# Kernel tuning notes

Hardware: AMD Instinct MI355X
Metric: run time of the kernel (lower is better)

## Reference

```python
import math
import jax, jax.numpy as jnp
import numpy as np

B, V, N, D, H = 8, 8, 1000, 256, 8
KS = D // H
TANH_CLIP = 10.0
F_NODE = 8   # node dynamic features incl. is_to_be_delivered flag
F_VEH = 8


def setup_inputs() -> dict:
    key = jax.random.key(0)
    ks = jax.random.split(key, 13)
    s = 1.0 / math.sqrt(D)
    mask = jax.random.uniform(ks[8], (B, V, N)) > 0.3
    mask = mask.at[:, :, 0].set(True)  # guarantee at least one feasible action
    return {
        'node_embeddings': jax.random.normal(ks[0], (B, N, D), jnp.float32),
        'fixed_context': jax.random.normal(ks[1], (B, 1, D), jnp.float32),
        'prev_node_embeddings': jax.random.normal(ks[2], (B, V, D), jnp.float32),
        'node_dynamic_features': jax.random.uniform(ks[3], (B, V, N, F_NODE), jnp.float32),
        'vehicle_dynamic_features': jax.random.uniform(ks[4], (B, V, F_VEH), jnp.float32),
        'glimpse_V_static': jax.random.normal(ks[5], (H, B, 1, N, KS), jnp.float32),
        'glimpse_K_static': jax.random.normal(ks[6], (H, B, 1, N, KS), jnp.float32),
        'logit_K_static': jax.random.normal(ks[7], (B, 1, N, D), jnp.float32),
        'feasibility_mask': mask,
        'pcs_weight': jax.random.normal(ks[9], (D, D + F_VEH), jnp.float32) * s,
        'pns1_weight': jax.random.normal(ks[10], (3 * D, F_NODE - 1), jnp.float32) * s,
        'pns2_weight': jax.random.normal(ks[11], (3 * D, 3 * D + 1), jnp.float32) * s,
        'po_weight': jax.random.normal(ks[12], (D, D), jnp.float32) * s,
    }


def _make_heads(x):
    # [B,V,N,D] -> [H,B,V,N,KS]  (matches unsqueeze/view/permute in torch code)
    b, v, n, _ = x.shape
    return x.reshape(b, v, n, H, KS).transpose(3, 0, 1, 2, 4)


def reference(node_embeddings, fixed_context, prev_node_embeddings,
              node_dynamic_features, vehicle_dynamic_features,
              glimpse_V_static, glimpse_K_static, logit_K_static,
              feasibility_mask, pcs_weight, pns1_weight, pns2_weight, po_weight):
    b, n, d = node_embeddings.shape
    v = vehicle_dynamic_features.shape[1]

    # projected current vehicle state
    cvs = jnp.concatenate([prev_node_embeddings, vehicle_dynamic_features], axis=-1)  # [B,V,D+Fv]
    proj_cvs = cvs @ pcs_weight.T                                                     # [B,V,D]

    # node dynamic embeddings (hypernet linears)
    flag = node_dynamic_features[..., -1:]
    feats = node_dynamic_features[..., :-1]
    x = feats @ pns1_weight.T                                   # [B,V,N,3D]
    x_ = jnp.concatenate([x, flag], axis=-1) @ pns2_weight.T    # [B,V,N,3D]
    nde = x + x_
    gVd, gKd, lKd = jnp.split(nde, 3, axis=-1)                  # each [B,V,N,D]

    glimpse_V = glimpse_V_static + _make_heads(gVd)             # [H,B,V,N,KS]
    glimpse_K = glimpse_K_static + _make_heads(gKd)             # [H,B,V,N,KS]
    logit_K = logit_K_static + lKd                              # [B,V,N,D]

    query = fixed_context + proj_cvs                            # [B,V,D]
    gQ = query.reshape(b, v, H, 1, KS).transpose(2, 0, 1, 3, 4)  # [H,B,V,1,KS]

    logmask = jnp.log(feasibility_mask.astype(jnp.float32))     # 0 / -inf, [B,V,N]

    compat = jnp.einsum('hbvqk,hbvnk->hbvqn', gQ, glimpse_K) / math.sqrt(KS)
    compat = compat + logmask[None, :, :, None, :]              # [H,B,V,1,N]

    # softmax over all (vehicle, node) pairs jointly
    attn = jax.nn.softmax(compat.reshape(H, b, v * n), axis=-1).reshape(compat.shape)
    heads = jnp.einsum('hbvqn,hbvnk->hbvqk', attn, glimpse_V)   # [H,B,V,1,KS]

    concated = heads.transpose(1, 2, 3, 0, 4).reshape(b, v, 1, d)
    final_Q = concated @ po_weight.T                            # [B,V,1,D]

    logits = jnp.einsum('bvqd,bvnd->bvqn', final_Q, logit_K) / math.sqrt(d)
    logits = jnp.tanh(logits) * TANH_CLIP
    logits = logits[:, :, 0, :] + logmask                       # [B,V,N]
    logits = logits.reshape(b, v * n)
    probs = jax.nn.softmax(logits, axis=1)

    # greedy (eval-mode) selection
    op = jnp.argmax(probs, axis=-1)
    prob = jnp.max(probs, axis=-1)
    logprob = jnp.log(prob)
    entropy = -jnp.sum(prob * logprob)
    selected_vecs = (op // n).astype(jnp.int64)
    selected_nodes = op % n
    return selected_vecs, selected_nodes, logprob, entropy
```

## Files before the change

kernel.cpp:

```cpp
#include <hip/hip_runtime.h>
#include <math.h>

#define OFF_MW     0
#define OFF_QUERY  6144
#define OFF_CSUMP  22528
#define OFF_HSTATP 23040
#define OFF_S8P    154112
#define OFF_FQ     186880
#define OFF_LQM    203264
#define OFF_EXPSP  203776
#define OFF_PACKP  204032
#define OFF_DONE   204544
#define OFF_BM     204545

__device__ inline float waveSum(float v){
  #pragma unroll
  for (int o = 32; o > 0; o >>= 1) v += __shfl_down(v, o, 64);
  return v;
}
__device__ inline unsigned long long waveMaxU(unsigned long long v){
  #pragma unroll
  for (int o = 32; o > 0; o >>= 1) {
    unsigned long long w = __shfl_down(v, o, 64);
    v = (w > v) ? w : v;
  }
  return v;
}
__device__ inline unsigned encF(float f){
  unsigned u = __float_as_uint(f);
  return (u & 0x80000000u) ? ~u : (u | 0x80000000u);
}
__device__ inline float decF(unsigned u){
  return (u & 0x80000000u) ? __uint_as_float(u & 0x7fffffffu)
                           : __uint_as_float(~u);
}

__global__ __launch_bounds__(256) void k_prep(
    const float* __restrict__ pns1, const float* __restrict__ pns2,
    const float* __restrict__ prev, const float* __restrict__ veh,
    const float* __restrict__ fixedc, const float* __restrict__ pcs,
    const void* __restrict__ maskp, float* __restrict__ W)
{
  int blk = blockIdx.x, tid = threadIdx.x;
  float* mw     = W + OFF_MW;
  float* queryp = W + OFF_QUERY;

  if (blk < 768) {
    int i = blk;
    __shared__ float red[28];
    const float* row = pns2 + (size_t)i * 769;
    float acc[7] = {0.f,0.f,0.f,0.f,0.f,0.f,0.f};
    #pragma unroll
    for (int t = 0; t < 3; t++) {
      int j = tid + 256 * t;
      float r = row[j];
      const float* w = pns1 + j * 7;
      #pragma unroll
      for (int f = 0; f < 7; f++) acc[f] += r * w[f];
    }
    #pragma unroll
    for (int f = 0; f < 7; f++) {
      float v = waveSum(acc[f]);
      if ((tid & 63) == 0) red[(tid >> 6) * 7 + f] = v;
    }
    __syncthreads();
    if (tid < 7) {
      float s = red[tid] + red[7 + tid] + red[14 + tid] + red[21 + tid];
      mw[i * 8 + tid] = pns1[i * 7 + tid] + s;
    } else if (tid == 7) {
      mw[i * 8 + 7] = row[768];
    }
  } else if (blk < 832) {
    int bv = blk - 768;
    __shared__ __align__(16) float cvs[264];
    cvs[tid] = prev[(size_t)bv * 256 + tid];
    if (tid < 8) cvs[256 + tid] = veh[bv * 8 + tid];
    __syncthreads();
    int b = bv >> 3;
    float a = fixedc[b * 256 + tid];
    const float4* c4 = (const float4*)cvs;
    const float4* w4 = (const float4*)(pcs + (size_t)tid * 264);
    #pragma unroll 8
    for (int k = 0; k < 66; k++) {
      float4 cv = c4[k], wv = w4[k];
      a += cv.x*wv.x + cv.y*wv.y + cv.z*wv.z + cv.w*wv.w;
    }
    queryp[(size_t)bv * 256 + tid] = a;
  } else {
    __shared__ unsigned hits[4];
    const unsigned char* mb = (const unsigned char*)maskp;
    bool hit = (tid > 0) && ((tid & 3) != 0) && (mb[tid] != 0);
    unsigned long long bal = __ballot(hit);
    if ((tid & 63) == 0) hits[tid >> 6] = (bal != 0ull) ? 1u : 0u;
    __syncthreads();
    if (tid == 0) {
      ((unsigned*)(W + OFF_BM))[0] = hits[0] | hits[1] | hits[2] | hits[3];
      ((unsigned*)(W + OFF_DONE))[0] = 0u;
    }
  }
}

__global__ __launch_bounds__(256) void k_attn(
    const float* __restrict__ node_dyn, const float* __restrict__ gVs,
    const float* __restrict__ gKs, const void* __restrict__ maskp,
    float* __restrict__ W)
{
  const int blk = blockIdx.x, tid = threadIdx.x;
  const int b = blk & 7, c = (blk >> 3) & 7, h = blk >> 6;
  const int n0 = c * 125;
  const float* mw     = W + OFF_MW;
  const float* queryp = W + OFF_QUERY;
  float* csum_p  = W + OFF_CSUMP;
  float* hstat_p = W + OFF_HSTATP;
  float* s8_p    = W + OFF_S8P;
  const int bytemode = *(const int*)(W + OFF_BM);

  __shared__ __align__(16) float p[1000];
  __shared__ __align__(16) float gq[256];
  __shared__ float mwK[256];
  __shared__ float qmk[64];
  __shared__ float red4[4];
  __shared__ float s8part[256];
  __shared__ __align__(16) float gvL[4000];
  __shared__ __align__(16) float gkL[4500];
  __shared__ __align__(16) float ndL[8000];

  gq[tid]  = queryp[(size_t)(b * 8 + (tid >> 5)) * 256 + h * 32 + (tid & 31)];
  mwK[tid] = mw[(256 + h * 32) * 8 + tid];
  __syncthreads();
  if (tid < 64) {
    int v = tid >> 3, f = tid & 7;
    float a = 0.f;
    #pragma unroll
    for (int k = 0; k < 32; k++)
      a += gq[v * 32 + k] * mwK[k * 8 + f];
    qmk[tid] = a;
  }
  {
    const float4* gv4 = (const float4*)(gVs + ((size_t)(h * 8 + b) * 1000 + n0) * 32);
    const float4* gk4 = (const float4*)(gKs + ((size_t)(h * 8 + b) * 1000 + n0) * 32);
    for (int idx = tid; idx < 1000; idx += 256) {
      int row = idx >> 3, c4 = idx & 7;
      ((float4*)gvL)[idx] = gv4[idx];
      ((float4*)(gkL + row * 36))[c4] = gk4[idx];
    }
  }
  __syncthreads();

  float tsum = 0.f;
  for (int e = tid; e < 1000; e += 256) {
    int v = e / 125;
    int i = e - v * 125;
    int n = n0 + i;
    int bvn = (b * 8 + v) * 1000 + n;
    const float4* nd4 = (const float4*)(node_dyn + (size_t)bvn * 8);
    float4 ndA = nd4[0], ndB = nd4[1];
    ((float4*)ndL)[e * 2]     = ndA;
    ((float4*)ndL)[e * 2 + 1] = ndB;
    const float4* gk4 = (const float4*)(gkL + i * 36);
    const float4* gq4 = (const float4*)(gq + v * 32);
    float s = 0.f;
    #pragma unroll
    for (int k4 = 0; k4 < 8; k4++) {
      float4 g = gk4[k4], q = gq4[k4];
      s += g.x*q.x + g.y*q.y + g.z*q.z + g.w*q.w;
    }
    const float* qm = qmk + v * 8;
    float dyn = ndA.x*qm[0] + ndA.y*qm[1] + ndA.z*qm[2] + ndA.w*qm[3]
              + ndB.x*qm[4] + ndB.y*qm[5] + ndB.z*qm[6] + ndB.w*qm[7];
    bool on = bytemode ? (((const unsigned char*)maskp)[bvn] != 0)
                       : (((const int*)maskp)[bvn] != 0);
    float cc = (s + dyn) * 0.17677669529663687f + (on ? 0.f : -INFINITY);
    float pv = __expf(cc);
    p[e] = pv;
    tsum += pv;
  }
  tsum = waveSum(tsum);
  if ((tid & 63) == 0) red4[tid >> 6] = tsum;
  __syncthreads();
  if (tid == 0) csum_p[blk] = red4[0] + red4[1] + red4[2] + red4[3];

  if (tid < 64) {
    int v = tid >> 3, kq = tid & 7;
    const float* pr = p + v * 125;
    const float4* gv4 = ((const float4*)gvL) + kq;
    float4 a = make_float4(0.f, 0.f, 0.f, 0.f);
    #pragma unroll 5
    for (int i = 0; i < 125; i++) {
      float pi = pr[i];
      float4 g = gv4[i * 8];
      a.x += pi * g.x; a.y += pi * g.y; a.z += pi * g.z; a.w += pi * g.w;
    }
    ((float4*)(hstat_p + (size_t)blk * 256))[tid] = a;
  } else {
    int j0 = tid - 64;
    #pragma unroll
    for (int rep = 0; rep < 2; rep++) {
      int t = j0 + rep * 192;
      if (t < 256) {
        int sidx = t & 3, vf = t >> 2;
        int v = vf >> 3, f = vf & 7;
        int i0 = sidx * 32;
        int iN = (sidx == 3) ? 29 : 32;
        const float* nd = ndL + ((size_t)(v * 125 + i0)) * 8 + f;
        const float* pr = p + v * 125 + i0;
        float a = 0.f;
        for (int i = 0; i < iN; i++) a += pr[i] * nd[i * 8];
        s8part[sidx * 64 + vf] = a;
      }
    }
  }
  __syncthreads();
  if (tid < 64)
    s8_p[(size_t)blk * 64 + tid] = s8part[tid] + s8part[64 + tid]
                                 + s8part[128 + tid] + s8part[192 + tid];
}

__global__ __launch_bounds__(256) void k_fq(
    const float* __restrict__ po, float* __restrict__ W)
{
  const int blk = blockIdx.x, tid = threadIdx.x;
  const int b = blk & 7, v = (blk >> 3) & 7;
  const float* mwgV    = W + OFF_MW;
  const float* mwgL    = W + OFF_MW + 512 * 8;
  const float* csum_p  = W + OFF_CSUMP;
  const float* hstat_p = W + OFF_HSTATP;
  const float* s8_p    = W + OFF_S8P;
  float* fqg  = W + OFF_FQ;
  float* lqmg = W + OFF_LQM;

  __shared__ __align__(16) float hstatF[2048];
  __shared__ float csumF[8];
  __shared__ float s8F[512];
  __shared__ __align__(16) float cl[256];
  __shared__ float fql[256];
  __shared__ float part[256];

  #pragma unroll
  for (int h2 = 0; h2 < 8; h2++) {
    float s = 0.f;
    #pragma unroll
    for (int cc = 0; cc < 8; cc++)
      s += hstat_p[(size_t)((h2 << 6) | (cc << 3) | b) * 256 + tid];
    hstatF[h2 * 256 + tid] = s;
  }
  if (tid < 8) {
    float s = 0.f;
    #pragma unroll
    for (int cc = 0; cc < 8; cc++) s += csum_p[(tid << 6) | (cc << 3) | b];
    csumF[tid] = s;
  }
  #pragma unroll
  for (int idx = tid; idx < 512; idx += 256) {
    int h2 = idx >> 6, vf = idx & 63;
    float s = 0.f;
    #pragma unroll
    for (int cc = 0; cc < 8; cc++)
      s += s8_p[(size_t)((h2 << 6) | (cc << 3) | b) * 64 + vf];
    s8F[idx] = s;
  }
  __syncthreads();
  {
    int h2 = tid >> 5, k2 = tid & 31;
    float dyn = 0.f;
    const float* s8pp = s8F + h2 * 64 + v * 8;
    const float* mwp = mwgV + tid * 8;
    #pragma unroll
    for (int f = 0; f < 8; f++) dyn += s8pp[f] * mwp[f];
    cl[tid] = (hstatF[h2 * 256 + v * 32 + k2] + dyn) / csumF[h2];
  }
  __syncthreads();
  {
    float a = 0.f;
    const float4* c4 = (const float4*)cl;
    const float4* w4 = (const float4*)(po + (size_t)tid * 256);
    #pragma unroll 8
    for (int e = 0; e < 64; e++) {
      float4 cv = c4[e], wv = w4[e];
      a += cv.x*wv.x + cv.y*wv.y + cv.z*wv.z + cv.w*wv.w;
    }
    fql[tid] = a;
    fqg[(size_t)(b * 8 + v) * 256 + tid] = a;
  }
  __syncthreads();
  {
    int cc2 = tid >> 3, f = tid & 7;
    float s = 0.f;
    for (int d = cc2 * 8; d < cc2 * 8 + 8; d++) s += fql[d] * mwgL[d * 8 + f];
    part[tid] = s;
  }
  __syncthreads();
  if (tid < 8) {
    float s = 0.f;
    for (int cc2 = 0; cc2 < 32; cc2++) s += part[cc2 * 8 + tid];
    lqmg[(b * 8 + v) * 8 + tid] = s;
  }
}

__global__ __launch_bounds__(256) void k_logits(
    const float* __restrict__ lKs, const float* __restrict__ node_dyn,
    const void* __restrict__ maskp, float* __restrict__ W,
    float* __restrict__ out)
{
  const int blk = blockIdx.x, tid = threadIdx.x;
  const int b = blk & 7, slice = blk >> 3;
  const int nn = tid >> 3, v = tid & 7;
  const int n = slice * 32 + nn;
  const bool valid = (n < 1000);
  const int n_c = valid ? n : 999;
  const float* fqg  = W + OFF_FQ;
  const float* lqmg = W + OFF_LQM;
  float* expsum_p = W + OFF_EXPSP;
  unsigned long long* packed_p = (unsigned long long*)(W + OFF_PACKP);
  unsigned* done = (unsigned*)(W + OFF_DONE);
  const int bytemode = *(const int*)(W + OFF_BM);

  __shared__ __align__(16) float bkL[32 * 260];
  __shared__ float red4[4];
  __shared__ unsigned long long rP[4];
  __shared__ unsigned ticket;

  {
    const float4* src = (const float4*)(lKs + (size_t)b * 1000 * 256);
    for (int idx = tid; idx < 2048; idx += 256) {
      int row = idx >> 6, d4 = idx & 63;
      int ng = slice * 32 + row; if (ng > 999) ng = 999;
      ((float4*)(bkL + row * 260))[d4] = src[(size_t)ng * 64 + d4];
    }
  }
  __syncthreads();

  int bvn = (b * 8 + v) * 1000 + n_c;
  const float4* A  = (const float4*)(fqg + (size_t)(b * 8 + v) * 256);
  const float4* Bk = (const float4*)(bkL + nn * 260);
  float s = 0.f;
  #pragma unroll 8
  for (int d4 = 0; d4 < 64; d4++) {
    float4 x = A[d4], y = Bk[d4];
    s += x.x*y.x + x.y*y.y + x.z*y.z + x.w*y.w;
  }
  const float4* nd4 = (const float4*)(node_dyn + (size_t)bvn * 8);
  float4 na = nd4[0], nb = nd4[1];
  const float* qm = lqmg + (b * 8 + v) * 8;
  float dyn = na.x*qm[0] + na.y*qm[1] + na.z*qm[2] + na.w*qm[3]
            + nb.x*qm[4] + nb.y*qm[5] + nb.z*qm[6] + nb.w*qm[7];
  float z = (s + dyn) * 0.0625f;
  bool on = bytemode ? (((const unsigned char*)maskp)[bvn] != 0)
                     : (((const int*)maskp)[bvn] != 0);
  float L = tanhf(z) * 10.0f + (on ? 0.f : -INFINITY);
  if (!valid) L = -INFINITY;
  float ex = __expf(L);
  unsigned idx = (unsigned)(v * 1000 + n_c);
  unsigned long long pk = ((unsigned long long)encF(L) << 32) | (unsigned)(~idx);
  float sEx = waveSum(ex);
  unsigned long long mP = waveMaxU(pk);
  if ((tid & 63) == 0) { red4[tid >> 6] = sEx; rP[tid >> 6] = mP; }
  __syncthreads();
  if (tid == 0) {
    float S = red4[0] + red4[1] + red4[2] + red4[3];
    unsigned long long P = rP[0];
    #pragma unroll
    for (int i = 1; i < 4; i++) P = (rP[i] > P) ? rP[i] : P;
    atomicExch(&expsum_p[blk], S);
    atomicExch(&packed_p[blk], P);
    __threadfence();
    ticket = atomicAdd(done, 1u);
  }
  __syncthreads();
  if (ticket == 255) {
    __threadfence();
    if (tid < 64) {
      float cEnt = 0.f;
      if (tid < 8) {
        float S = 0.f;
        unsigned long long P = 0ull;
        for (int sl = 0; sl < 32; sl++) {
          int j = sl * 8 + tid;
          S += atomicAdd(&expsum_p[j], 0.0f);
          unsigned long long q = atomicAdd(&packed_p[j], 0ull);
          P = (q > P) ? q : P;
        }
        float best = decF((unsigned)(P >> 32));
        unsigned bi = ~(unsigned)(P & 0xffffffffu);
        float logprob = best - logf(S);
        float prob = __expf(logprob);
        out[tid]      = (float)(bi / 1000);
        out[8 + tid]  = (float)(bi % 1000);
        out[16 + tid] = logprob;
        cEnt = prob * logprob;
      }
      cEnt = waveSum(cEnt);
      if (tid == 0) out[24] = -cEnt;
    }
  }
}

extern "C" void kernel_launch(void* const* d_in, const int* in_sizes, int n_in,
                              void* d_out, int out_size, void* d_ws, size_t ws_size,
                              hipStream_t stream) {
  const float* fixedc   = (const float*)d_in[1];
  const float* prev     = (const float*)d_in[2];
  const float* node_dyn = (const float*)d_in[3];
  const float* veh      = (const float*)d_in[4];
  const float* gVs      = (const float*)d_in[5];
  const float* gKs      = (const float*)d_in[6];
  const float* lKs      = (const float*)d_in[7];
  const void*  mask     = d_in[8];
  const float* pcs      = (const float*)d_in[9];
  const float* pns1     = (const float*)d_in[10];
  const float* pns2     = (const float*)d_in[11];
  const float* po       = (const float*)d_in[12];
  float* W   = (float*)d_ws;
  float* out = (float*)d_out;

  k_prep<<<833, 256, 0, stream>>>(pns1, pns2, prev, veh, fixedc, pcs, mask, W);
  k_attn<<<512, 256, 0, stream>>>(node_dyn, gVs, gKs, mask, W);
  k_fq<<<64, 256, 0, stream>>>(po, W);
  k_logits<<<256, 256, 0, stream>>>(lKs, node_dyn, mask, W, out);
}
```

Baseline: 142.8 us.

## Fuse final-query projection into logits kernel, recomputing per block

Removes the separate k_fq launch. Each logits block now reduces the head partials for its batch and computes the po projection and the logit-side dynamic query for all 8 vehicles in shared memory. This drops one kernel launch and the global round trip for fq/lqm. In exchange every one of the 32 slice blocks per batch redoes the 8x256x256 projection and rereads po, adding redundant compute, memory traffic and shared memory use (about 60KB) per block.

```diff
diff --git a/kernel.cpp b/kernel.cpp
--- a/kernel.cpp
+++ b/kernel.cpp
@@ -6,8 +6,6 @@
 #define OFF_CSUMP  22528
 #define OFF_HSTATP 23040
 #define OFF_S8P    154112
-#define OFF_FQ     186880
-#define OFF_LQM    203264
 #define OFF_EXPSP  203776
 #define OFF_PACKP  204032
 #define OFF_DONE   204544
@@ -216,91 +214,10 @@
                                  + s8part[128 + tid] + s8part[192 + tid];
 }
 
-__global__ __launch_bounds__(256) void k_fq(
-    const float* __restrict__ po, float* __restrict__ W)
-{
-  const int blk = blockIdx.x, tid = threadIdx.x;
-  const int b = blk & 7, v = (blk >> 3) & 7;
-  const float* mwgV    = W + OFF_MW;
-  const float* mwgL    = W + OFF_MW + 512 * 8;
-  const float* csum_p  = W + OFF_CSUMP;
-  const float* hstat_p = W + OFF_HSTATP;
-  const float* s8_p    = W + OFF_S8P;
-  float* fqg  = W + OFF_FQ;
-  float* lqmg = W + OFF_LQM;
-
-  __shared__ __align__(16) float hstatF[2048];
-  __shared__ float csumF[8];
-  __shared__ float s8F[512];
-  __shared__ __align__(16) float cl[256];
-  __shared__ float fql[256];
-  __shared__ float part[256];
-
-  #pragma unroll
-  for (int h2 = 0; h2 < 8; h2++) {
-    float s = 0.f;
-    #pragma unroll
-    for (int cc = 0; cc < 8; cc++)
-      s += hstat_p[(size_t)((h2 << 6) | (cc << 3) | b) * 256 + tid];
-    hstatF[h2 * 256 + tid] = s;
-  }
-  if (tid < 8) {
-    float s = 0.f;
-    #pragma unroll
-    for (int cc = 0; cc < 8; cc++) s += csum_p[(tid << 6) | (cc << 3) | b];
-    csumF[tid] = s;
-  }
-  #pragma unroll
-  for (int idx = tid; idx < 512; idx += 256) {
-    int h2 = idx >> 6, vf = idx & 63;
-    float s = 0.f;
-    #pragma unroll
-    for (int cc = 0; cc < 8; cc++)
-      s += s8_p[(size_t)((h2 << 6) | (cc << 3) | b) * 64 + vf];
-    s8F[idx] = s;
-  }
-  __syncthreads();
-  {
-    int h2 = tid >> 5, k2 = tid & 31;
-    float dyn = 0.f;
-    const float* s8pp = s8F + h2 * 64 + v * 8;
-    const float* mwp = mwgV + tid * 8;
-    #pragma unroll
-    for (int f = 0; f < 8; f++) dyn += s8pp[f] * mwp[f];
-    cl[tid] = (hstatF[h2 * 256 + v * 32 + k2] + dyn) / csumF[h2];
-  }
-  __syncthreads();
-  {
-    float a = 0.f;
-    const float4* c4 = (const float4*)cl;
-    const float4* w4 = (const float4*)(po + (size_t)tid * 256);
-    #pragma unroll 8
-    for (int e = 0; e < 64; e++) {
-      float4 cv = c4[e], wv = w4[e];
-      a += cv.x*wv.x + cv.y*wv.y + cv.z*wv.z + cv.w*wv.w;
-    }
-    fql[tid] = a;
-    fqg[(size_t)(b * 8 + v) * 256 + tid] = a;
-  }
-  __syncthreads();
-  {
-    int cc2 = tid >> 3, f = tid & 7;
-    float s = 0.f;
-    for (int d = cc2 * 8; d < cc2 * 8 + 8; d++) s += fql[d] * mwgL[d * 8 + f];
-    part[tid] = s;
-  }
-  __syncthreads();
-  if (tid < 8) {
-    float s = 0.f;
-    for (int cc2 = 0; cc2 < 32; cc2++) s += part[cc2 * 8 + tid];
-    lqmg[(b * 8 + v) * 8 + tid] = s;
-  }
-}
-
 __global__ __launch_bounds__(256) void k_logits(
     const float* __restrict__ lKs, const float* __restrict__ node_dyn,
-    const void* __restrict__ maskp, float* __restrict__ W,
-    float* __restrict__ out)
+    const void* __restrict__ maskp, const float* __restrict__ po,
+    float* __restrict__ W, float* __restrict__ out)
 {
   const int blk = blockIdx.x, tid = threadIdx.x;
   const int b = blk & 7, slice = blk >> 3;
@@ -308,14 +225,23 @@
   const int n = slice * 32 + nn;
   const bool valid = (n < 1000);
   const int n_c = valid ? n : 999;
-  const float* fqg  = W + OFF_FQ;
-  const float* lqmg = W + OFF_LQM;
+  const float* mwgV    = W + OFF_MW;
+  const float* mwgL    = W + OFF_MW + 512 * 8;
+  const float* csum_p  = W + OFF_CSUMP;
+  const float* hstat_p = W + OFF_HSTATP;
+  const float* s8_p    = W + OFF_S8P;
   float* expsum_p = W + OFF_EXPSP;
   unsigned long long* packed_p = (unsigned long long*)(W + OFF_PACKP);
   unsigned* done = (unsigned*)(W + OFF_DONE);
   const int bytemode = *(const int*)(W + OFF_BM);
 
   __shared__ __align__(16) float bkL[32 * 260];
+  __shared__ __align__(16) float clL[8 * 256];
+  __shared__ __align__(16) float fqlL[8 * 260];
+  __shared__ float s8F[512];
+  __shared__ float csumF[8];
+  __shared__ float mwLL[2048];
+  __shared__ float lqmF[64];
   __shared__ float red4[4];
   __shared__ unsigned long long rP[4];
   __shared__ unsigned ticket;
@@ -328,10 +254,85 @@
       ((float4*)(bkL + row * 260))[d4] = src[(size_t)ng * 64 + d4];
     }
   }
+  for (int idx = tid; idx < 512; idx += 256) {
+    int h2 = idx >> 6, vf = idx & 63;
+    float s = 0.f;
+    #pragma unroll
+    for (int cc = 0; cc < 8; cc++)
+      s += s8_p[(size_t)((h2 << 6) | (cc << 3) | b) * 64 + vf];
+    s8F[idx] = s;
+  }
+  if (tid < 8) {
+    float s = 0.f;
+    #pragma unroll
+    for (int cc = 0; cc < 8; cc++) s += csum_p[(tid << 6) | (cc << 3) | b];
+    csumF[tid] = s;
+  }
+  for (int idx = tid; idx < 2048; idx += 256) mwLL[idx] = mwgL[idx];
+  float hac[8];
+  {
+    const int h2 = tid >> 5, k2 = tid & 31;
+    #pragma unroll
+    for (int v2 = 0; v2 < 8; v2++) hac[v2] = 0.f;
+    #pragma unroll
+    for (int cc = 0; cc < 8; cc++) {
+      const float* hp = hstat_p + (size_t)((tid >> 5 << 6) | (cc << 3) | b) * 256;
+      #pragma unroll
+      for (int v2 = 0; v2 < 8; v2++) hac[v2] += hp[v2 * 32 + k2];
+    }
+    (void)h2;
+  }
+  __syncthreads();
+  {
+    const int h2 = tid >> 5;
+    float mwr[8];
+    const float* mwp = mwgV + tid * 8;
+    #pragma unroll
+    for (int f = 0; f < 8; f++) mwr[f] = mwp[f];
+    float inv = csumF[h2];
+    #pragma unroll
+    for (int v2 = 0; v2 < 8; v2++) {
+      float dyn = 0.f;
+      const float* s8pp = s8F + h2 * 64 + v2 * 8;
+      #pragma unroll
+      for (int f = 0; f < 8; f++) dyn += s8pp[f] * mwr[f];
+      clL[v2 * 256 + tid] = (hac[v2] + dyn) / inv;
+    }
+  }
+  __syncthreads();
+  {
+    float acc[8];
+    #pragma unroll
+    for (int v2 = 0; v2 < 8; v2++) acc[v2] = 0.f;
+    const float4* w4 = (const float4*)(po + (size_t)tid * 256);
+    #pragma unroll 4
+    for (int e = 0; e < 64; e++) {
+      float4 wv = w4[e];
+      #pragma unroll
+      for (int v2 = 0; v2 < 8; v2++) {
+        float4 cv = ((const float4*)(clL + v2 * 256))[e];
+        acc[v2] += cv.x*wv.x + cv.y*wv.y + cv.z*wv.z + cv.w*wv.w;
+      }
+    }
+    #pragma unroll
+    for (int v2 = 0; v2 < 8; v2++) fqlL[v2 * 260 + tid] = acc[v2];
+  }
+  __syncthreads();
+  if (tid < 64) {
+    int v2 = tid >> 3, f = tid & 7;
+    const float* fr = fqlL + v2 * 260;
+    float s = 0.f;
+    for (int cc2 = 0; cc2 < 32; cc2++) {
+      float p2 = 0.f;
+      for (int d = cc2 * 8; d < cc2 * 8 + 8; d++) p2 += fr[d] * mwLL[d * 8 + f];
+      s += p2;
+    }
+    lqmF[tid] = s;
+  }
   __syncthreads();
 
   int bvn = (b * 8 + v) * 1000 + n_c;
-  const float4* A  = (const float4*)(fqg + (size_t)(b * 8 + v) * 256);
+  const float4* A  = (const float4*)(fqlL + v * 260);
   const float4* Bk = (const float4*)(bkL + nn * 260);
   float s = 0.f;
   #pragma unroll 8
@@ -341,7 +342,7 @@
   }
   const float4* nd4 = (const float4*)(node_dyn + (size_t)bvn * 8);
   float4 na = nd4[0], nb = nd4[1];
-  const float* qm = lqmg + (b * 8 + v) * 8;
+  const float* qm = lqmF + v * 8;
   float dyn = na.x*qm[0] + na.y*qm[1] + na.z*qm[2] + na.w*qm[3]
             + nb.x*qm[4] + nb.y*qm[5] + nb.z*qm[6] + nb.w*qm[7];
   float z = (s + dyn) * 0.0625f;
@@ -415,6 +416,5 @@
 
   k_prep<<<833, 256, 0, stream>>>(pns1, pns2, prev, veh, fixedc, pcs, mask, W);
   k_attn<<<512, 256, 0, stream>>>(node_dyn, gVs, gKs, mask, W);
-  k_fq<<<64, 256, 0, stream>>>(po, W);
-  k_logits<<<256, 256, 0, stream>>>(lKs, node_dyn, mask, W, out);
-}
+  k_logits<<<256, 256, 0, stream>>>(lKs, node_dyn, mask, po, W, out);
+}
```

Result: faster. 139.1 us (-2.6%).
